# Kernel optimization log

Hardware: AMD Instinct MI355X
Metric: run time of the kernel (lower is better)

## Reference

```python
import jax, jax.numpy as jnp
import numpy as np

B, S, D = 4, 4096, 1024
H, F = 16, 256
HD = D // H  # 64


def setup_inputs() -> dict:
    key = jax.random.key(0)
    ks = jax.random.split(key, 10)
    scale = 1.0 / np.sqrt(D)
    x = jax.random.normal(ks[0], (B, S, D), dtype=jnp.float32)
    Wq = jax.random.normal(ks[1], (D, D), dtype=jnp.float32) * scale
    bq = jnp.zeros((D,), dtype=jnp.float32)
    Wk = jax.random.normal(ks[2], (D, D), dtype=jnp.float32) * scale
    bk = jnp.zeros((D,), dtype=jnp.float32)
    Wv = jax.random.normal(ks[3], (D, D), dtype=jnp.float32) * scale
    bv = jnp.zeros((D,), dtype=jnp.float32)
    Wo = jax.random.normal(ks[4], (D, D), dtype=jnp.float32) * scale
    bo = jnp.zeros((D,), dtype=jnp.float32)
    rf = jax.random.normal(ks[5], (H, HD, F), dtype=jnp.float32) / np.sqrt(F)
    return {"x": x, "Wq": Wq, "bq": bq, "Wk": Wk, "bk": bk,
            "Wv": Wv, "bv": bv, "Wo": Wo, "bo": bo, "rf": rf}


def _heads(y):
    # [B,S,D] -> [B,H,S,HD]
    return y.reshape(B, S, H, HD).transpose(0, 2, 1, 3)


def reference(x, Wq, bq, Wk, bk, Wv, bv, Wo, bo, rf):
    q = _heads(x @ Wq.T + bq)
    k = _heads(x @ Wk.T + bk)
    v = _heads(x @ Wv.T + bv)
    # positive feature maps: softplus(random projection)
    q_prime = jax.nn.softplus(jnp.einsum('bhsd,hdf->bhsf', q, rf))
    k_prime = jax.nn.softplus(jnp.einsum('bhsd,hdf->bhsf', k, rf))
    kv = jnp.einsum('bhsf,bhsd->bhfd', k_prime, v)          # [B,H,F,HD]
    k_sum = k_prime.sum(axis=2)                              # [B,H,F]
    qkv = jnp.einsum('bhsf,bhfd->bhsd', q_prime, kv)        # [B,H,S,HD]
    denom = jnp.einsum('bhsf,bhf->bhs', q_prime, k_sum) + 1e-8
    out = qkv / denom[..., None]
    out = out.transpose(0, 2, 1, 3).reshape(B, S, D)
    return out @ Wo.T + bo
```

## Files before the change

kernel.cpp:

```cpp
#include <hip/hip_runtime.h>
#include <hip/hip_bf16.h>
#include <math.h>

#define Bb 4
#define Ss 4096
#define Dd 1024
#define Hh 16
#define Ff 256
#define HDd 64
#define Mm (Bb*Ss)

typedef unsigned int u32;
typedef unsigned short u16;

typedef __attribute__((ext_vector_type(8))) short bf16x8;
typedef __attribute__((ext_vector_type(4))) float f32x4;

__device__ __forceinline__ float bflo(u32 u){ union{u32 i; float f;} c; c.i = u << 16; return c.f; }
__device__ __forceinline__ float bfhi(u32 u){ union{u32 i; float f;} c; c.i = u & 0xffff0000u; return c.f; }
__device__ __forceinline__ u16 f2b(float f){
  union{float f; u32 i;} c; c.f = f;
  u32 x = c.i;
  return (u16)((x + 0x7fffu + ((x >> 16) & 1u)) >> 16);
}
__device__ __forceinline__ u32 pk2(float lo, float hi){
  union { __hip_bfloat162 h; u32 u; } c;
  c.h = __float22bfloat162_rn(make_float2(lo, hi));
  return c.u;
}
__device__ __forceinline__ float sfast(float x){
  return fmaxf(x, 0.f) + __logf(1.f + __expf(-fabsf(x)));
}
__device__ __forceinline__ void gload_lds16(const u16* g, u16* l){
  __builtin_amdgcn_global_load_lds(
      (const __attribute__((address_space(1))) void*)g,
      (__attribute__((address_space(3))) void*)l, 16, 0, 0);
}

__global__ void cvt_bf16(const float* __restrict__ in, u16* __restrict__ out, int n)
{
  int i = (blockIdx.x * 256 + threadIdx.x) * 8;
  if (i >= n) return;
  float4 a = *reinterpret_cast<const float4*>(in + i);
  float4 b = *reinterpret_cast<const float4*>(in + i + 4);
  *reinterpret_cast<uint4*>(out + i) =
      make_uint4(pk2(a.x, a.y), pk2(a.z, a.w), pk2(b.x, b.y), pk2(b.z, b.w));
}

__global__ void zero_f32(float* __restrict__ p, int n)
{
  int i = blockIdx.x * 256 + threadIdx.x;
  if (i < n) p[i] = 0.f;
}

template<typename OT, bool BROW>
__global__ __launch_bounds__(256, 2) void mfma_gemm_bt(
    const u16* __restrict__ A, const u16* __restrict__ W,
    const float* __restrict__ bias, OT* __restrict__ C,
    int M, int N, int K)
{
  __shared__ __align__(16) u16 As[128 * 32];
  __shared__ __align__(16) u16 Bs[128 * 32];

  const int tid = threadIdx.x;
  const int wave = tid >> 6, lane = tid & 63;
  const int quad = lane >> 4, lm = lane & 15;
  const int wm = (wave >> 1) * 64, wn = (wave & 1) * 64;
  const int m0 = blockIdx.x * 128, n0 = blockIdx.y * 128;

  f32x4 acc[4][4] = {};

  for (int k0 = 0; k0 < K; k0 += 32) {
#pragma unroll
    for (int j = 0; j < 2; j++) {
      const int c = wave * 128 + j * 64 + lane;
      const int r = c >> 2, cg = c & 3;
      u16* ldsA = &As[(wave * 128 + j * 64) * 8];
      u16* ldsB = &Bs[(wave * 128 + j * 64) * 8];
      gload_lds16(A + (size_t)(m0 + r) * K + k0 + cg * 8, ldsA);
      gload_lds16(W + (size_t)(n0 + r) * K + k0 + cg * 8, ldsB);
    }
    __syncthreads();

    bf16x8 af[4], bf[4];
#pragma unroll
    for (int mi = 0; mi < 4; mi++)
      af[mi] = *reinterpret_cast<const bf16x8*>(&As[(wm + mi * 16 + lm) * 32 + quad * 8]);
#pragma unroll
    for (int ni = 0; ni < 4; ni++)
      bf[ni] = *reinterpret_cast<const bf16x8*>(&Bs[(wn + ni * 16 + lm) * 32 + quad * 8]);
#pragma unroll
    for (int mi = 0; mi < 4; mi++)
#pragma unroll
      for (int ni = 0; ni < 4; ni++)
        acc[mi][ni] = __builtin_amdgcn_mfma_f32_16x16x32_bf16(af[mi], bf[ni], acc[mi][ni], 0, 0, 0);
    __syncthreads();
  }

#pragma unroll
  for (int mi = 0; mi < 4; mi++)
#pragma unroll
    for (int ni = 0; ni < 4; ni++) {
      const int n = n0 + wn + ni * 16 + lm;
      const float bvn = BROW ? 0.f : bias[n];
#pragma unroll
      for (int r = 0; r < 4; r++) {
        const int m = m0 + wm + mi * 16 + quad * 4 + r;
        const float val = acc[mi][ni][r] + (BROW ? bias[m] : bvn);
        if constexpr (sizeof(OT) == 2) ((u16*)C)[(size_t)m * N + n] = f2b(val);
        else                           ((float*)C)[(size_t)m * N + n] = val;
      }
    }
}

__global__ void rf_transpose(const float* __restrict__ rf, float* __restrict__ rft)
{
  const int h = blockIdx.x, d = blockIdx.y, f = threadIdx.x;
  rft[((size_t)h * Ff + f) * HDd + d] = rf[((size_t)(h * HDd + d)) * Ff + f];
}

#define NSPLIT 8
#define SCHUNKS (Ss / NSPLIT / 64)

__global__ __launch_bounds__(256, 2) void kv_fused(
    const u16* __restrict__ Km, const u16* __restrict__ Vt,
    const float* __restrict__ rft, float* __restrict__ kv, float* __restrict__ ksum)
{
  __shared__ __align__(16) u16 RF[Ff * 64];
  __shared__ __align__(16) u16 KS[64 * 64];
  __shared__ __align__(16) u16 VS[64 * 64];
  __shared__ __align__(16) u16 PT[4][64 * 64];

  const int bh = blockIdx.x;
  const int b = bh >> 4, h = bh & 15;
  const int s0 = blockIdx.y * (Ss / NSPLIT);
  const int tid = threadIdx.x;
  const int wave = tid >> 6, lane = tid & 63;
  const int quad = lane >> 4, lm = lane & 15;
  const int F0 = wave * 64;

  {
    const float* rh = rft + (size_t)h * Ff * HDd;
#pragma unroll
    for (int i = 0; i < 8; i++) {
      int qq = tid + 256 * i;
      int r = qq >> 3, c = qq & 7;
      const float* src = rh + r * 64 + c * 8;
      float4 a = *reinterpret_cast<const float4*>(src);
      float4 e = *reinterpret_cast<const float4*>(src + 4);
      *reinterpret_cast<uint4*>((char*)RF + r * 128 + ((c ^ (r & 7)) * 16)) =
          make_uint4(pk2(a.x, a.y), pk2(a.z, a.w), pk2(e.x, e.y), pk2(e.z, e.w));
    }
  }

  f32x4 kvacc[4][4] = {};
  float kss[4] = {0.f, 0.f, 0.f, 0.f};

  for (int ch = 0; ch < SCHUNKS; ch++) {
    const int sc0 = s0 + ch * 64;
#pragma unroll
    for (int i = 0; i < 2; i++) {
      int qq = tid + 256 * i;
      int r = qq >> 3, c = qq & 7;
      uint4 kd = *reinterpret_cast<const uint4*>(
          Km + (size_t)(b * Ss + sc0 + r) * Dd + h * 64 + c * 8);
      *reinterpret_cast<uint4*>((char*)KS + r * 128 + ((c ^ (r & 7)) * 16)) = kd;
      uint4 vd = *reinterpret_cast<const uint4*>(
          Vt + (size_t)(h * 64 + r) * Mm + b * Ss + sc0 + c * 8);
      *reinterpret_cast<uint4*>((char*)VS + r * 128 + ((c ^ (r & 7)) * 16)) = vd;
    }
    __syncthreads();

    f32x4 p[4][4] = {};
#pragma unroll
    for (int ks = 0; ks < 2; ks++) {
      bf16x8 af[4], bfr[4];
#pragma unroll
      for (int mi = 0; mi < 4; mi++) {
        int row = mi * 16 + lm;
        af[mi] = *reinterpret_cast<const bf16x8*>(
            (char*)KS + row * 128 + (((ks * 4 + quad) ^ (row & 7)) * 16));
      }
#pragma unroll
      for (int ni = 0; ni < 4; ni++) {
        int row = ni * 16 + lm;
        bfr[ni] = *reinterpret_cast<const bf16x8*>(
            (char*)RF + (F0 + row) * 128 + (((ks * 4 + quad) ^ (row & 7)) * 16));
      }
#pragma unroll
      for (int mi = 0; mi < 4; mi++)
#pragma unroll
        for (int ni = 0; ni < 4; ni++)
          p[mi][ni] = __builtin_amdgcn_mfma_f32_16x16x32_bf16(af[mi], bfr[ni], p[mi][ni], 0, 0, 0);
    }

#pragma unroll
    for (int mi = 0; mi < 4; mi++)
#pragma unroll
      for (int ni = 0; ni < 4; ni++) {
        float v0 = sfast(p[mi][ni][0]);
        float v1 = sfast(p[mi][ni][1]);
        float v2 = sfast(p[mi][ni][2]);
        float v3 = sfast(p[mi][ni][3]);
        kss[ni] += (v0 + v1) + (v2 + v3);
        int row = ni * 16 + lm;
        int off = (row * 128 + mi * 32 + quad * 8) ^ ((row & 7) << 4);
        *reinterpret_cast<uint2*>((char*)&PT[wave][0] + off) =
            make_uint2(pk2(v0, v1), pk2(v2, v3));
      }

#pragma unroll
    for (int ks = 0; ks < 2; ks++) {
      bf16x8 a2[4], b2[4];
#pragma unroll
      for (int mi = 0; mi < 4; mi++) {
        int row = mi * 16 + lm;
        a2[mi] = *reinterpret_cast<const bf16x8*>(
            (char*)&PT[wave][0] + row * 128 + (((ks * 4 + quad) ^ (row & 7)) * 16));
      }
#pragma unroll
      for (int ni = 0; ni < 4; ni++) {
        int row = ni * 16 + lm;
        b2[ni] = *reinterpret_cast<const bf16x8*>(
            (char*)VS + row * 128 + (((ks * 4 + quad) ^ (row & 7)) * 16));
      }
#pragma unroll
      for (int mi = 0; mi < 4; mi++)
#pragma unroll
        for (int ni = 0; ni < 4; ni++)
          kvacc[mi][ni] = __builtin_amdgcn_mfma_f32_16x16x32_bf16(a2[mi], b2[ni], kvacc[mi][ni], 0, 0, 0);
    }
    __syncthreads();
  }

  float* kvp = kv + (size_t)bh * Ff * HDd;
#pragma unroll
  for (int mi = 0; mi < 4; mi++)
#pragma unroll
    for (int ni = 0; ni < 4; ni++)
#pragma unroll
      for (int rr = 0; rr < 4; rr++) {
        int f = F0 + mi * 16 + quad * 4 + rr;
        int d = ni * 16 + lm;
        atomicAdd(kvp + (size_t)f * HDd + d, kvacc[mi][ni][rr]);
      }
#pragma unroll
  for (int ni = 0; ni < 4; ni++) {
    float v = kss[ni];
    v += __shfl_xor(v, 16, 64);
    v += __shfl_xor(v, 32, 64);
    if (quad == 0) atomicAdd(ksum + (size_t)bh * Ff + F0 + ni * 16 + lm, v);
  }
}

__global__ void kvt_cvt(const float* __restrict__ kv, u16* __restrict__ kvtb)
{
  const int bh = blockIdx.x;
  const int d = threadIdx.x & 63, fg = threadIdx.x >> 6;
  const float* src = kv + (size_t)bh * Ff * HDd + d;
  u32* dst = reinterpret_cast<u32*>(kvtb + (size_t)bh * HDd * Ff + (size_t)d * Ff + fg * 64);
#pragma unroll
  for (int j = 0; j < 32; j++) {
    float v0 = src[(size_t)(fg * 64 + 2 * j) * HDd];
    float v1 = src[(size_t)(fg * 64 + 2 * j + 1) * HDd];
    dst[j] = pk2(v0, v1);
  }
}

#define ASPLIT 16
#define ACHUNKS (Ss / ASPLIT / 64)

__global__ __launch_bounds__(256, 2) void attn_fused(
    const u16* __restrict__ Qm, const float* __restrict__ rft,
    const u16* __restrict__ kvtb, const float* __restrict__ ksum,
    u16* __restrict__ attnb)
{
  __shared__ __align__(16) u16 P4[4][64 * 64];
  __shared__ __align__(16) float den4[64][4];

  const int bh = blockIdx.x;
  const int b = bh >> 4, h = bh & 15;
  const int s0 = blockIdx.y * (Ss / ASPLIT);
  const int tid = threadIdx.x;
  const int wave = tid >> 6, lane = tid & 63;
  const int quad = lane >> 4, lm = lane & 15;
  const int F0 = wave * 64;

  bf16x8 bfr[4][2];
  {
    const float* rh = rft + (size_t)h * Ff * HDd;
#pragma unroll
    for (int ni = 0; ni < 4; ni++) {
      const float* rrow = rh + (size_t)(F0 + ni * 16 + lm) * HDd;
#pragma unroll
      for (int ks = 0; ks < 2; ks++) {
        float4 a = *reinterpret_cast<const float4*>(rrow + ks * 32 + quad * 8);
        float4 e = *reinterpret_cast<const float4*>(rrow + ks * 32 + quad * 8 + 4);
        union { u32 w[4]; bf16x8 v; } u;
        u.w[0] = pk2(a.x, a.y); u.w[1] = pk2(a.z, a.w);
        u.w[2] = pk2(e.x, e.y); u.w[3] = pk2(e.z, e.w);
        bfr[ni][ks] = u.v;
      }
    }
  }
  bf16x8 b2r[4][2];
  {
    const u16* kb = kvtb + (size_t)bh * HDd * Ff + (size_t)(wave * 16 + lm) * Ff;
#pragma unroll
    for (int fb = 0; fb < 4; fb++)
#pragma unroll
      for (int k2 = 0; k2 < 2; k2++)
        b2r[fb][k2] = *reinterpret_cast<const bf16x8*>(kb + fb * 64 + k2 * 32 + quad * 8);
  }
  float ksv[4];
#pragma unroll
  for (int ni = 0; ni < 4; ni++)
    ksv[ni] = ksum[(size_t)bh * Ff + F0 + ni * 16 + lm];

  for (int ch = 0; ch < ACHUNKS; ch++) {
    const int sc0 = s0 + ch * 64;

    bf16x8 af[4][2];
#pragma unroll
    for (int mi = 0; mi < 4; mi++) {
      const u16* qrow = Qm + (size_t)(b * Ss + sc0 + mi * 16 + lm) * Dd + h * 64;
#pragma unroll
      for (int ks = 0; ks < 2; ks++)
        af[mi][ks] = *reinterpret_cast<const bf16x8*>(qrow + ks * 32 + quad * 8);
    }
    f32x4 p[4][4] = {};
#pragma unroll
    for (int ks = 0; ks < 2; ks++)
#pragma unroll
      for (int mi = 0; mi < 4; mi++)
#pragma unroll
        for (int ni = 0; ni < 4; ni++)
          p[mi][ni] = __builtin_amdgcn_mfma_f32_16x16x32_bf16(af[mi][ks], bfr[ni][ks], p[mi][ni], 0, 0, 0);

#pragma unroll
    for (int mi = 0; mi < 4; mi++) {
      const int sbase = mi * 16 + quad * 4;
      float dd[4] = {0.f, 0.f, 0.f, 0.f};
#pragma unroll
      for (int ni = 0; ni < 4; ni++) {
        u32 pk01 = pk2(sfast(p[mi][ni][0]), sfast(p[mi][ni][1]));
        u32 pk23 = pk2(sfast(p[mi][ni][2]), sfast(p[mi][ni][3]));
        dd[0] += bflo(pk01) * ksv[ni];
        dd[1] += bfhi(pk01) * ksv[ni];
        dd[2] += bflo(pk23) * ksv[ni];
        dd[3] += bfhi(pk23) * ksv[ni];
        u32 ob01 = (u32)__shfl_xor((int)pk01, 1, 64);
        u32 ob23 = (u32)__shfl_xor((int)pk23, 1, 64);
        const int odd = lm & 1;
        u32 w_a = odd ? ((ob23 & 0xffffu) | (pk23 << 16))
                      : ((pk01 & 0xffffu) | (ob01 << 16));
        u32 w_b = odd ? ((ob23 >> 16)     | (pk23 & 0xffff0000u))
                      : ((pk01 >> 16)     | (ob01 & 0xffff0000u));
        const int row_a = sbase + (odd ? 2 : 0);
        const int row_b = sbase + (odd ? 3 : 1);
        const int fpb = ni * 16 + (lm & ~1);
        const int cc = fpb >> 3;
        const int bib = (fpb & 7) * 2;
        *reinterpret_cast<u32*>((char*)&P4[wave][0] + row_a * 128 + ((cc ^ (row_a & 7)) << 4) + bib) = w_a;
        *reinterpret_cast<u32*>((char*)&P4[wave][0] + row_b * 128 + ((cc ^ (row_b & 7)) << 4) + bib) = w_b;
      }
#pragma unroll
      for (int r = 0; r < 4; r++) {
        float v = dd[r];
        v += __shfl_xor(v, 1, 64);
        v += __shfl_xor(v, 2, 64);
        v += __shfl_xor(v, 4, 64);
        v += __shfl_xor(v, 8, 64);
        if (lm == 0) den4[sbase + r][wave] = v;
      }
    }
    __syncthreads();

    f32x4 acc2[4] = {};
#pragma unroll
    for (int fb = 0; fb < 4; fb++)
#pragma unroll
      for (int k2 = 0; k2 < 2; k2++) {
        bf16x8 af2[4];
#pragma unroll
        for (int mi = 0; mi < 4; mi++) {
          int row = mi * 16 + lm;
          af2[mi] = *reinterpret_cast<const bf16x8*>(
              (char*)&P4[fb][0] + row * 128 + (((k2 * 4 + quad) ^ (row & 7)) << 4));
        }
#pragma unroll
        for (int mi = 0; mi < 4; mi++)
          acc2[mi] = __builtin_amdgcn_mfma_f32_16x16x32_bf16(af2[mi], b2r[fb][k2], acc2[mi], 0, 0, 0);
      }

#pragma unroll
    for (int mi = 0; mi < 4; mi++) {
#pragma unroll
      for (int r = 0; r < 4; r++) {
        const int s = mi * 16 + quad * 4 + r;
        float4 dv = *reinterpret_cast<const float4*>(&den4[s][0]);
        const float inv = 1.f / ((dv.x + dv.y) + (dv.z + dv.w) + 1e-8f);
        attnb[(size_t)(b * Ss + sc0 + s) * Dd + h * 64 + wave * 16 + lm] =
            f2b(acc2[mi][r] * inv);
      }
    }
    __syncthreads();
  }
}

extern "C" void kernel_launch(void* const* d_in, const int* in_sizes, int n_in,
                              void* d_out, int out_size, void* d_ws, size_t ws_size,
                              hipStream_t stream)
{
  const float* x  = (const float*)d_in[0];
  const float* Wq = (const float*)d_in[1];
  const float* bq = (const float*)d_in[2];
  const float* Wk = (const float*)d_in[3];
  const float* bk = (const float*)d_in[4];
  const float* Wv = (const float*)d_in[5];
  const float* bv = (const float*)d_in[6];
  const float* Wo = (const float*)d_in[7];
  const float* bo = (const float*)d_in[8];
  const float* rf = (const float*)d_in[9];

  char* w = (char*)d_ws;
  u16* xb = (u16*)w;        w += (size_t)Mm * Dd * 2;
  u16* q  = (u16*)w;        w += (size_t)Mm * Dd * 2;
  u16* k  = (u16*)w;        w += (size_t)Mm * Dd * 2;
  u16* vt = (u16*)w;        w += (size_t)Mm * Dd * 2;
  u16* wqb = (u16*)w;       w += (size_t)Dd * Dd * 2;
  u16* wkb = (u16*)w;       w += (size_t)Dd * Dd * 2;
  u16* wvb = (u16*)w;       w += (size_t)Dd * Dd * 2;
  u16* wob = (u16*)w;       w += (size_t)Dd * Dd * 2;
  float* kv = (float*)w;    w += (size_t)(Bb * Hh) * Ff * HDd * 4;
  float* ks = (float*)w;    w += (size_t)(Bb * Hh) * Ff * 4;
  float* rft = (float*)w;   w += (size_t)Hh * Ff * HDd * 4;
  u16* kvtb = wqb;

  cvt_bf16<<<(Mm * Dd / 8 + 255) / 256, 256, 0, stream>>>(x, xb, Mm * Dd);
  cvt_bf16<<<(Dd * Dd / 8 + 255) / 256, 256, 0, stream>>>(Wq, wqb, Dd * Dd);
  cvt_bf16<<<(Dd * Dd / 8 + 255) / 256, 256, 0, stream>>>(Wk, wkb, Dd * Dd);
  cvt_bf16<<<(Dd * Dd / 8 + 255) / 256, 256, 0, stream>>>(Wv, wvb, Dd * Dd);
  cvt_bf16<<<(Dd * Dd / 8 + 255) / 256, 256, 0, stream>>>(Wo, wob, Dd * Dd);

  const int nz = (Bb * Hh) * Ff * HDd + (Bb * Hh) * Ff;
  zero_f32<<<(nz + 255) / 256, 256, 0, stream>>>(kv, nz);
  rf_transpose<<<dim3(Hh, HDd), 256, 0, stream>>>(rf, rft);

  const dim3 gg(Mm / 128, Dd / 128);
  mfma_gemm_bt<u16, false><<<gg, 256, 0, stream>>>(xb, wqb, bq, q, Mm, Dd, Dd);
  mfma_gemm_bt<u16, false><<<gg, 256, 0, stream>>>(xb, wkb, bk, k, Mm, Dd, Dd);
  const dim3 gv(Dd / 128, Mm / 128);
  mfma_gemm_bt<u16, true><<<gv, 256, 0, stream>>>(wvb, xb, bv, vt, Dd, Mm, Dd);

  kv_fused<<<dim3(Bb * Hh, NSPLIT), 256, 0, stream>>>(k, vt, rft, kv, ks);

  kvt_cvt<<<Bb * Hh, 256, 0, stream>>>(kv, kvtb);

  attn_fused<<<dim3(Bb * Hh, ASPLIT), 256, 0, stream>>>(q, rft, kvtb, ks, xb);

  mfma_gemm_bt<float, false><<<gg, 256, 0, stream>>>(xb, wob, bo, (float*)d_out, Mm, Dd, Dd);
}
```

Before: 509.4 us.

## Double-buffer K/V tiles with direct global-to-LDS loads in kv_fused

The kv_fused kernel now stages K and V chunks into two LDS buffers using direct global-to-LDS loads, prefetching the next chunk while computing the current one, with explicit vmcnt waits and raw barriers. The random-feature matrix is held in registers per wave instead of being staged in LDS, which frees LDS for the second buffer. The aim is to hide global load latency behind the MFMA work and remove LDS reads of the RF tile, at the cost of more register pressure and hand-managed synchronization. This relies on the gload_lds16 helper, which is expected to be defined in the part of the file not shown.

```diff
diff --git a/kernel.cpp b/kernel.cpp
--- a/kernel.cpp
+++ b/kernel.cpp
@@ -126,9 +126,8 @@
     const u16* __restrict__ Km, const u16* __restrict__ Vt,
     const float* __restrict__ rft, float* __restrict__ kv, float* __restrict__ ksum)
 {
-  __shared__ __align__(16) u16 RF[Ff * 64];
-  __shared__ __align__(16) u16 KS[64 * 64];
-  __shared__ __align__(16) u16 VS[64 * 64];
+  __shared__ __align__(16) u16 KSd[2][64 * 64];
+  __shared__ __align__(16) u16 VSd[2][64 * 64];
   __shared__ __align__(16) u16 PT[4][64 * 64];
 
   const int bh = blockIdx.x;
@@ -139,59 +138,71 @@
   const int quad = lane >> 4, lm = lane & 15;
   const int F0 = wave * 64;
 
+  bf16x8 bfr[4][2];
   {
     const float* rh = rft + (size_t)h * Ff * HDd;
 #pragma unroll
-    for (int i = 0; i < 8; i++) {
-      int qq = tid + 256 * i;
-      int r = qq >> 3, c = qq & 7;
-      const float* src = rh + r * 64 + c * 8;
-      float4 a = *reinterpret_cast<const float4*>(src);
-      float4 e = *reinterpret_cast<const float4*>(src + 4);
-      *reinterpret_cast<uint4*>((char*)RF + r * 128 + ((c ^ (r & 7)) * 16)) =
-          make_uint4(pk2(a.x, a.y), pk2(a.z, a.w), pk2(e.x, e.y), pk2(e.z, e.w));
-    }
-  }
+    for (int ni = 0; ni < 4; ni++) {
+      const float* rrow = rh + (size_t)(F0 + ni * 16 + lm) * HDd;
+#pragma unroll
+      for (int ks = 0; ks < 2; ks++) {
+        float4 a = *reinterpret_cast<const float4*>(rrow + ks * 32 + quad * 8);
+        float4 e = *reinterpret_cast<const float4*>(rrow + ks * 32 + quad * 8 + 4);
+        union { u32 w[4]; bf16x8 v; } u;
+        u.w[0] = pk2(a.x, a.y); u.w[1] = pk2(a.z, a.w);
+        u.w[2] = pk2(e.x, e.y); u.w[3] = pk2(e.z, e.w);
+        bfr[ni][ks] = u.v;
+      }
+    }
+  }
+
+  const int j0 = wave * 64 + lane, j1 = j0 + 256;
+  const int r0 = j0 >> 3, c0 = (j0 & 7) ^ (r0 & 7);
+  const int r1 = j1 >> 3, c1 = (j1 & 7) ^ (r1 & 7);
+
+  auto KV_STAGE = [&](int buf, int ch) {
+    const int sc = s0 + ch * 64;
+    gload_lds16(Km + (size_t)(b * Ss + sc + r0) * Dd + h * 64 + c0 * 8, &KSd[buf][(wave * 64) * 8]);
+    gload_lds16(Km + (size_t)(b * Ss + sc + r1) * Dd + h * 64 + c1 * 8, &KSd[buf][(wave * 64 + 256) * 8]);
+    gload_lds16(Vt + (size_t)(h * 64 + r0) * Mm + b * Ss + sc + c0 * 8, &VSd[buf][(wave * 64) * 8]);
+    gload_lds16(Vt + (size_t)(h * 64 + r1) * Mm + b * Ss + sc + c1 * 8, &VSd[buf][(wave * 64 + 256) * 8]);
+  };
 
   f32x4 kvacc[4][4] = {};
   float kss[4] = {0.f, 0.f, 0.f, 0.f};
 
+  KV_STAGE(0, 0);
+
+#pragma unroll
   for (int ch = 0; ch < SCHUNKS; ch++) {
-    const int sc0 = s0 + ch * 64;
-#pragma unroll
-    for (int i = 0; i < 2; i++) {
-      int qq = tid + 256 * i;
-      int r = qq >> 3, c = qq & 7;
-      uint4 kd = *reinterpret_cast<const uint4*>(
-          Km + (size_t)(b * Ss + sc0 + r) * Dd + h * 64 + c * 8);
-      *reinterpret_cast<uint4*>((char*)KS + r * 128 + ((c ^ (r & 7)) * 16)) = kd;
-      uint4 vd = *reinterpret_cast<const uint4*>(
-          Vt + (size_t)(h * 64 + r) * Mm + b * Ss + sc0 + c * 8);
-      *reinterpret_cast<uint4*>((char*)VS + r * 128 + ((c ^ (r & 7)) * 16)) = vd;
-    }
-    __syncthreads();
+    const int cur = ch & 1;
+    if (ch + 1 < SCHUNKS) {
+      KV_STAGE(cur ^ 1, ch + 1);
+      asm volatile("s_waitcnt vmcnt(4)" ::: "memory");
+    } else {
+      asm volatile("s_waitcnt vmcnt(0)" ::: "memory");
+    }
+    __builtin_amdgcn_s_barrier();
+    __builtin_amdgcn_sched_barrier(0);
+
+    const u16* KSc = &KSd[cur][0];
+    const u16* VSc = &VSd[cur][0];
 
     f32x4 p[4][4] = {};
 #pragma unroll
-    for (int ks = 0; ks < 2; ks++) {
-      bf16x8 af[4], bfr[4];
+    for (int ks2 = 0; ks2 < 2; ks2++) {
+      bf16x8 af[4];
 #pragma unroll
       for (int mi = 0; mi < 4; mi++) {
         int row = mi * 16 + lm;
         af[mi] = *reinterpret_cast<const bf16x8*>(
-            (char*)KS + row * 128 + (((ks * 4 + quad) ^ (row & 7)) * 16));
-      }
-#pragma unroll
-      for (int ni = 0; ni < 4; ni++) {
-        int row = ni * 16 + lm;
-        bfr[ni] = *reinterpret_cast<const bf16x8*>(
-            (char*)RF + (F0 + row) * 128 + (((ks * 4 + quad) ^ (row & 7)) * 16));
+            (const char*)KSc + row * 128 + (((ks2 * 4 + quad) ^ (row & 7)) * 16));
       }
 #pragma unroll
       for (int mi = 0; mi < 4; mi++)
 #pragma unroll
         for (int ni = 0; ni < 4; ni++)
-          p[mi][ni] = __builtin_amdgcn_mfma_f32_16x16x32_bf16(af[mi], bfr[ni], p[mi][ni], 0, 0, 0);
+          p[mi][ni] = __builtin_amdgcn_mfma_f32_16x16x32_bf16(af[mi], bfr[ni][ks2], p[mi][ni], 0, 0, 0);
     }
 
 #pragma unroll
@@ -210,19 +221,19 @@
       }
 
 #pragma unroll
-    for (int ks = 0; ks < 2; ks++) {
+    for (int ks2 = 0; ks2 < 2; ks2++) {
       bf16x8 a2[4], b2[4];
 #pragma unroll
       for (int mi = 0; mi < 4; mi++) {
         int row = mi * 16 + lm;
         a2[mi] = *reinterpret_cast<const bf16x8*>(
-            (char*)&PT[wave][0] + row * 128 + (((ks * 4 + quad) ^ (row & 7)) * 16));
+            (char*)&PT[wave][0] + row * 128 + (((ks2 * 4 + quad) ^ (row & 7)) * 16));
       }
 #pragma unroll
       for (int ni = 0; ni < 4; ni++) {
         int row = ni * 16 + lm;
         b2[ni] = *reinterpret_cast<const bf16x8*>(
-            (char*)VS + row * 128 + (((ks * 4 + quad) ^ (row & 7)) * 16));
+            (const char*)VSc + row * 128 + (((ks2 * 4 + quad) ^ (row & 7)) * 16));
       }
 #pragma unroll
       for (int mi = 0; mi < 4; mi++)
@@ -230,7 +241,9 @@
         for (int ni = 0; ni < 4; ni++)
           kvacc[mi][ni] = __builtin_amdgcn_mfma_f32_16x16x32_bf16(a2[mi], b2[ni], kvacc[mi][ni], 0, 0, 0);
     }
-    __syncthreads();
+
+    __builtin_amdgcn_sched_barrier(0);
+    __builtin_amdgcn_s_barrier();
   }
 
   float* kvp = kv + (size_t)bh * Ff * HDd;
```

After: 568.7 us. 11.7% more time.
